# Performance work log

Measured on AMD Instinct MI355X. Metric: run time of the kernel, lower is better.

## Reference

```python
import jax, jax.numpy as jnp
import numpy as np

B, T, DIM = 8, 1024, 512
H, DK, L = 8, 64, 32          # heads, dim_key, rel_pos_length
DH = H * DK                    # dim_hidden = 512
DOUT = 512
EPS = 1e-5


def setup_inputs() -> dict:
    key = jax.random.key(0)
    ks = jax.random.split(key, 5)
    x = jax.random.normal(ks[0], (B, T, DIM), jnp.float32)
    Wqkv = jax.random.normal(ks[1], (3 * DH, DIM), jnp.float32) * (1.0 / np.sqrt(DIM))
    Wout = jax.random.normal(ks[2], (DOUT, DH), jnp.float32) * (1.0 / np.sqrt(DH))
    bout = jax.random.normal(ks[3], (DOUT,), jnp.float32) * 0.01
    rel_positions = jax.random.normal(ks[4], (2 * L - 1, DK), jnp.float32)
    bn_gamma = jnp.ones((DK,), jnp.float32)
    bn_beta = jnp.zeros((DK,), jnp.float32)
    return {"x": x, "Wqkv": Wqkv, "Wout": Wout, "bout": bout,
            "rel_positions": rel_positions, "bn_gamma": bn_gamma, "bn_beta": bn_beta}


def reference(x, Wqkv, Wout, bout, rel_positions, bn_gamma, bn_beta):
    b, t, f = x.shape
    # Conv1d(dim, 3*dim_hidden, 1, bias=False) on x.transpose(1,2) == pointwise matmul
    qkv = jnp.einsum('btf,of->bot', x, Wqkv)          # (b, 3*DH, t)
    q, k, v = jnp.split(qkv, 3, axis=1)
    q = q.reshape(b * H, DK, t)
    k = k.reshape(b * H, DK, t)
    v = v.reshape(b * H, DK, t)

    # linear-attention core: softmax over sequence for k, tiny DKxDK context
    k = jax.nn.softmax(k, axis=-1)
    context = jnp.einsum('ndt,net->nde', k, v)        # (n, DK, DK)
    content_out = jnp.einsum('nde,ndt->net', context, q)  # (n, DK, t); norm_queries=False

    # Relative-position path. Original builds one-hot It (t,t,2L-1) and
    # Pt = einsum('tir,rd->tid', It, rel_positions); then
    # St = einsum('ndt,tid->nit', q, Pt); rel = einsum('nit,net->net', St, v)
    #     = v * (sum_i St)[:,None,:].
    # sum_i Pt[t,i,d] = sum over valid band offsets of rel_positions -> band matmul.
    r = jnp.arange(-(L - 1), L)                       # (2L-1,)
    pos = jnp.arange(t)
    tgt = pos[:, None] + r[None, :]                   # i = x + r
    valid = ((tgt >= 0) & (tgt < t)).astype(x.dtype)  # (t, 2L-1)
    Psum = valid @ rel_positions                      # (t, DK) == Pt.sum(axis=1)
    S = jnp.einsum('ndt,td->nt', q, Psum)             # (n, t)
    rel = v * S[:, None, :]                           # (n, DK, t)

    # BatchNorm1d(DK), training-mode batch stats over (n, t), biased variance
    mu = jnp.mean(rel, axis=(0, 2), keepdims=True)
    var = jnp.mean((rel - mu) ** 2, axis=(0, 2), keepdims=True)
    rel = (rel - mu) * jax.lax.rsqrt(var + EPS) * bn_gamma[None, :, None] + bn_beta[None, :, None]

    out = (content_out + rel).reshape(b, DH, t)
    # Conv1d(dim_hidden, dim_out, 1) with bias
    return jnp.einsum('od,bdt->bot', Wout, out) + bout[None, :, None]
```

## Files before the change

### kernel.cpp

```cpp
#include <hip/hip_runtime.h>
#include <hip/hip_bf16.h>


typedef short bf16x8 __attribute__((ext_vector_type(8)));
typedef float f32x4 __attribute__((ext_vector_type(4)));

static __device__ __forceinline__ unsigned short f2bf(float f) {
  __hip_bfloat16 h = __float2bfloat16(f);
  return *reinterpret_cast<unsigned short*>(&h);
}
static __device__ __forceinline__ float bf2f(unsigned short u) {
  union { unsigned int i; float f; } c; c.i = ((unsigned int)u) << 16;
  return c.f;
}
static __device__ __forceinline__ void gl_lds16(const unsigned short* g, unsigned short* l) {
  __builtin_amdgcn_global_load_lds((const __attribute__((address_space(1))) unsigned int*)g,
                                   (__attribute__((address_space(3))) unsigned int*)l,
                                   16, 0, 0);
}

__global__ __launch_bounds__(256) void prep(const float* __restrict__ x,
                                            const float* __restrict__ wqkv,
                                            const float* __restrict__ wout,
                                            const float* __restrict__ relpos,
                                            unsigned short* __restrict__ xb,
                                            unsigned short* __restrict__ wqkvb,
                                            unsigned short* __restrict__ woutb,
                                            float* __restrict__ PsumT) {
  const int bx = blockIdx.x;
  if (bx < 5120) {
    int j = bx * 256 + threadIdx.x;
    const float* src; unsigned short* dst;
    if (j < 1048576) { src = x; dst = xb; }
    else if (j < 1245184) { j -= 1048576; src = wqkv; dst = wqkvb; }
    else { j -= 1245184; src = wout; dst = woutb; }
    float4 v = ((const float4*)src)[j];
    ushort4 o = {f2bf(v.x), f2bf(v.y), f2bf(v.z), f2bf(v.w)};
    ((ushort4*)dst)[j] = o;
  } else {
    const int idx = bx - 5120;
    const int d = idx >> 2;
    const int t = (idx & 3) * 256 + threadIdx.x;
    float acc = 0.f;
    for (int j = 0; j < 63; ++j) {
      int i = t + j - 31;
      float v = relpos[j * 64 + d];
      if (i >= 0 && i < 1024) acc += v;
    }
    PsumT[d * 1024 + t] = acc;
  }
}


__global__ __launch_bounds__(256) void gemm_qkv(const unsigned short* __restrict__ A,
                                                const unsigned short* __restrict__ B,
                                                unsigned short* __restrict__ C) {
  __shared__ alignas(16) unsigned short As[8192];
  __shared__ alignas(16) unsigned short Bs[8192];
  const int tid = threadIdx.x;
  const int wave = tid >> 6, lane = tid & 63;
  const int bm = blockIdx.y * 128, bn = blockIdx.x * 128;
  const int wm = (wave >> 1) * 64, wn = (wave & 1) * 64;
  const int fr = lane & 15, cq = lane >> 4;
  const unsigned short* srcA[4];
  const unsigned short* srcB[4];
#pragma unroll
  for (int j = 0; j < 4; ++j) {
    const int s = tid + j * 256;
    const int row = s >> 3, cp = s & 7;
    const int c = cp ^ (row & 7);
    srcA[j] = A + (size_t)(bm + row) * 512 + c * 8;
    srcB[j] = B + (size_t)(bn + row) * 512 + c * 8;
  }
  int offA[4][2], offB[4][2];
#pragma unroll
  for (int i = 0; i < 4; ++i)
#pragma unroll
    for (int ks = 0; ks < 2; ++ks) {
      int ra = wm + i * 16 + fr;
      offA[i][ks] = (ra * 8 + ((ks * 4 + cq) ^ (ra & 7))) * 8;
      int rb = wn + i * 16 + fr;
      offB[i][ks] = (rb * 8 + ((ks * 4 + cq) ^ (rb & 7))) * 8;
    }
  f32x4 acc[4][4];
#pragma unroll
  for (int i = 0; i < 4; ++i)
#pragma unroll
    for (int j = 0; j < 4; ++j) acc[i][j] = (f32x4){0.f, 0.f, 0.f, 0.f};
  for (int k0 = 0; k0 < 512; k0 += 64) {
    __syncthreads();
#pragma unroll
    for (int j = 0; j < 4; ++j) {
      gl_lds16(srcA[j] + k0, As + (wave * 64 + j * 256) * 8);
      gl_lds16(srcB[j] + k0, Bs + (wave * 64 + j * 256) * 8);
    }
    __builtin_amdgcn_s_waitcnt(0);
    __syncthreads();
#pragma unroll
    for (int ks = 0; ks < 2; ++ks) {
      bf16x8 af[4], bq[4];
#pragma unroll
      for (int mi = 0; mi < 4; ++mi) af[mi] = *(const bf16x8*)(As + offA[mi][ks]);
#pragma unroll
      for (int nj = 0; nj < 4; ++nj) bq[nj] = *(const bf16x8*)(Bs + offB[nj][ks]);
#pragma unroll
      for (int mi = 0; mi < 4; ++mi)
#pragma unroll
        for (int nj = 0; nj < 4; ++nj)
          acc[mi][nj] = __builtin_amdgcn_mfma_f32_16x16x32_bf16(af[mi], bq[nj], acc[mi][nj], 0, 0, 0);
    }
  }
#pragma unroll
  for (int mi = 0; mi < 4; ++mi) {
    const int row0 = bm + wm + mi * 16 + (lane >> 4) * 4;
#pragma unroll
    for (int nj = 0; nj < 4; ++nj) {
      const int col = bn + wn + nj * 16 + fr;
#pragma unroll
      for (int rr = 0; rr < 4; ++rr)
        C[(size_t)(row0 + rr) * 8192 + col] = f2bf(acc[mi][nj][rr]);
    }
  }
}

__global__ __launch_bounds__(256) void gemm_out(const unsigned short* __restrict__ A,
                                                const unsigned short* __restrict__ B,
                                                const float* __restrict__ bias,
                                                float* __restrict__ out) {
  __shared__ alignas(16) unsigned short As[8192];
  __shared__ alignas(16) unsigned short Bs[8192];
  const int tid = threadIdx.x;
  const int wave = tid >> 6, lane = tid & 63;
  const int bm = blockIdx.y * 128, bn = blockIdx.x * 128;
  const int wm = (wave >> 1) * 64, wn = (wave & 1) * 64;
  const int fr = lane & 15, cq = lane >> 4;
  const unsigned short* srcA[4];
  const unsigned short* srcB[4];
#pragma unroll
  for (int j = 0; j < 4; ++j) {
    const int s = tid + j * 256;
    const int row = s >> 3, cp = s & 7;
    const int c = cp ^ (row & 7);
    srcA[j] = A + (size_t)(bm + row) * 512 + c * 8;
    srcB[j] = B + (size_t)(bn + row) * 512 + c * 8;
  }
  int offA[4][2], offB[4][2];
#pragma unroll
  for (int i = 0; i < 4; ++i)
#pragma unroll
    for (int ks = 0; ks < 2; ++ks) {
      int ra = wm + i * 16 + fr;
      offA[i][ks] = (ra * 8 + ((ks * 4 + cq) ^ (ra & 7))) * 8;
      int rb = wn + i * 16 + fr;
      offB[i][ks] = (rb * 8 + ((ks * 4 + cq) ^ (rb & 7))) * 8;
    }
  f32x4 acc[4][4];
#pragma unroll
  for (int i = 0; i < 4; ++i)
#pragma unroll
    for (int j = 0; j < 4; ++j) acc[i][j] = (f32x4){0.f, 0.f, 0.f, 0.f};
  for (int k0 = 0; k0 < 512; k0 += 64) {
    __syncthreads();
#pragma unroll
    for (int j = 0; j < 4; ++j) {
      gl_lds16(srcA[j] + k0, As + (wave * 64 + j * 256) * 8);
      gl_lds16(srcB[j] + k0, Bs + (wave * 64 + j * 256) * 8);
    }
    __builtin_amdgcn_s_waitcnt(0);
    __syncthreads();
#pragma unroll
    for (int ks = 0; ks < 2; ++ks) {
      bf16x8 af[4], bq[4];
#pragma unroll
      for (int mi = 0; mi < 4; ++mi) af[mi] = *(const bf16x8*)(As + offA[mi][ks]);
#pragma unroll
      for (int nj = 0; nj < 4; ++nj) bq[nj] = *(const bf16x8*)(Bs + offB[nj][ks]);
#pragma unroll
      for (int mi = 0; mi < 4; ++mi)
#pragma unroll
        for (int nj = 0; nj < 4; ++nj)
          acc[mi][nj] = __builtin_amdgcn_mfma_f32_16x16x32_bf16(af[mi], bq[nj], acc[mi][nj], 0, 0, 0);
    }
  }
#pragma unroll
  for (int mi = 0; mi < 4; ++mi) {
    const int row0 = bm + wm + mi * 16 + (lane >> 4) * 4;
#pragma unroll
    for (int nj = 0; nj < 4; ++nj) {
      const int col = bn + wn + nj * 16 + fr;
      const int b = col >> 10, t = col & 1023;
#pragma unroll
      for (int rr = 0; rr < 4; ++rr)
        out[(size_t)b * 524288 + (size_t)(row0 + rr) * 1024 + t] = acc[mi][nj][rr] + bias[row0 + rr];
    }
  }
}

__global__ __launch_bounds__(256) void stats(const unsigned short* __restrict__ qkv,
                                             const float* __restrict__ PsumT,
                                             float* __restrict__ S,
                                             float* __restrict__ part1,
                                             float* __restrict__ part2,
                                             float* __restrict__ lse) {
  const int bx = blockIdx.x;
  const int tid = threadIdx.x, wave = tid >> 6, lane = tid & 63;
  __shared__ float swave[4][64];
  __shared__ float s_lds[64];
  if (bx < 1024) {
    const int tc = bx & 15, n = bx >> 4;
    const int b = n >> 3, h = n & 7;
    const int t0 = tc * 64;
    const int tg = lane & 7, rg = lane >> 3;
    const unsigned short* qbase = qkv + (size_t)(h * 64) * 8192 + b * 1024 + t0 + tg * 8;
    const float* pbase = PsumT + t0 + tg * 8;
    float acc[8] = {0.f};
#pragma unroll
    for (int i = 0; i < 2; ++i) {
      const int d = wave * 16 + i * 8 + rg;
      bf16x8 qv = *(const bf16x8*)(qbase + (size_t)d * 8192);
      float4 p0 = *(const float4*)(pbase + d * 1024);
      float4 p1 = *(const float4*)(pbase + d * 1024 + 4);
      float p[8] = {p0.x, p0.y, p0.z, p0.w, p1.x, p1.y, p1.z, p1.w};
#pragma unroll
      for (int j = 0; j < 8; ++j) acc[j] = fmaf(bf2f((unsigned short)qv[j]), p[j], acc[j]);
    }
#pragma unroll
    for (int off = 8; off < 64; off <<= 1)
#pragma unroll
      for (int j = 0; j < 8; ++j) acc[j] += __shfl_xor(acc[j], off);
    if (rg == 0) {
#pragma unroll
      for (int j = 0; j < 8; ++j) swave[wave][tg * 8 + j] = acc[j];
    }
    __syncthreads();
    if (tid < 64) {
      float s = swave[0][tid] + swave[1][tid] + swave[2][tid] + swave[3][tid];
      s_lds[tid] = s;
      S[(size_t)n * 1024 + t0 + tid] = s;
    }
    __syncthreads();
    const unsigned short* vbase = qkv + (size_t)(1024 + h * 64) * 8192 + b * 1024 + t0 + tg * 8;
    const int blk = n * 16 + tc;
    float sv[8];
#pragma unroll
    for (int j = 0; j < 8; ++j) sv[j] = s_lds[tg * 8 + j];
#pragma unroll
    for (int i = 0; i < 2; ++i) {
      const int e = wave * 16 + i * 8 + rg;
      bf16x8 vv = *(const bf16x8*)(vbase + (size_t)e * 8192);
      float a1 = 0.f, a2 = 0.f;
#pragma unroll
      for (int j = 0; j < 8; ++j) {
        float val = bf2f((unsigned short)vv[j]) * sv[j];
        a1 += val;
        a2 = fmaf(val, val, a2);
      }
#pragma unroll
      for (int off = 1; off < 8; off <<= 1) {
        a1 += __shfl_xor(a1, off);
        a2 += __shfl_xor(a2, off);
      }
      if (tg == 0) {
        part1[e * 1024 + blk] = a1;
        part2[e * 1024 + blk] = a2;
      }
    }
  } else {
    const int r = (bx - 1024) * 4 + wave;
    const int hd = r >> 3, b = r & 7;
    const unsigned short* row = qkv + (size_t)(512 + hd) * 8192 + b * 1024 + lane * 16;
    uint4 u0 = *(const uint4*)row;
    uint4 u1 = *(const uint4*)(row + 8);
    const unsigned short* us0 = (const unsigned short*)&u0;
    const unsigned short* us1 = (const unsigned short*)&u1;
    float f[16];
#pragma unroll
    for (int i = 0; i < 8; ++i) { f[i] = bf2f(us0[i]); f[8 + i] = bf2f(us1[i]); }
    float m = f[0];
#pragma unroll
    for (int i = 1; i < 16; ++i) m = fmaxf(m, f[i]);
#pragma unroll
    for (int off = 32; off; off >>= 1) m = fmaxf(m, __shfl_xor(m, off));
    float s = 0.f;
#pragma unroll
    for (int i = 0; i < 16; ++i) s += __expf(f[i] - m);
#pragma unroll
    for (int off = 32; off; off >>= 1) s += __shfl_xor(s, off);
    if (lane == 0) lse[r] = m + __logf(s);
  }
}

__global__ __launch_bounds__(256) void context_mfma(const unsigned short* __restrict__ qkv,
                                                    const float* __restrict__ lse,
                                                    float* __restrict__ ctx_part) {
  const int tc = blockIdx.x, n = blockIdx.y;
  const int b = n >> 3, h = n & 7;
  const int tid = threadIdx.x;
  const int wave = tid >> 6, lane = tid & 63;
  __shared__ float ls[64];
  __shared__ float ctx_l[64][68];
  if (tid < 64) ls[tid] = lse[(h * 64 + tid) * 8 + b];
  __syncthreads();
  const int fr = lane & 15, fk = (lane >> 4) * 8;
  const size_t colbase = (size_t)b * 1024 + tc * 256 + wave * 64;
  const unsigned short* kbase = qkv + (size_t)(512 + h * 64) * 8192 + colbase;
  const unsigned short* vbase = qkv + (size_t)(1024 + h * 64) * 8192 + colbase;
  f32x4 acc[4][4];
#pragma unroll
  for (int i = 0; i < 4; ++i)
#pragma unroll
    for (int j = 0; j < 4; ++j) acc[i][j] = (f32x4){0.f, 0.f, 0.f, 0.f};
#pragma unroll
  for (int ks = 0; ks < 2; ++ks) {
    const int tb = ks * 32 + fk;
    bf16x8 aF[4], bF[4];
#pragma unroll
    for (int dt = 0; dt < 4; ++dt) {
      const int row = dt * 16 + fr;
      bf16x8 kv = *(const bf16x8*)(kbase + (size_t)row * 8192 + tb);
      const float lv = ls[row];
      bf16x8 pv;
#pragma unroll
      for (int j = 0; j < 8; ++j)
        pv[j] = (short)f2bf(__expf(bf2f((unsigned short)kv[j]) - lv));
      aF[dt] = pv;
    }
#pragma unroll
    for (int et = 0; et < 4; ++et)
      bF[et] = *(const bf16x8*)(vbase + (size_t)(et * 16 + fr) * 8192 + tb);
#pragma unroll
    for (int dt = 0; dt < 4; ++dt)
#pragma unroll
      for (int et = 0; et < 4; ++et)
        acc[dt][et] = __builtin_amdgcn_mfma_f32_16x16x32_bf16(aF[dt], bF[et], acc[dt][et], 0, 0, 0);
  }
#pragma unroll
  for (int w = 0; w < 4; ++w) {
    if (wave == w) {
#pragma unroll
      for (int dt = 0; dt < 4; ++dt)
#pragma unroll
        for (int et = 0; et < 4; ++et) {
          const int col = et * 16 + fr;
#pragma unroll
          for (int rr = 0; rr < 4; ++rr) {
            const int rw = dt * 16 + (lane >> 4) * 4 + rr;
            if (w == 0) ctx_l[rw][col] = acc[dt][et][rr];
            else ctx_l[rw][col] += acc[dt][et][rr];
          }
        }
    }
    __syncthreads();
  }
  float* outp = ctx_part + ((size_t)tc * 64 + n) * 4096;
  for (int i = tid * 4; i < 4096; i += 1024) {
    const int rw = i >> 6, cc = i & 63;
    *(float4*)(outp + i) = *(const float4*)&ctx_l[rw][cc];
  }
}

__global__ __launch_bounds__(256) void reduce2(const float* __restrict__ part,
                                               float* __restrict__ ctx,
                                               const float* __restrict__ part1,
                                               const float* __restrict__ part2,
                                               const float* __restrict__ gamma,
                                               const float* __restrict__ beta,
                                               float* __restrict__ scale,
                                               float* __restrict__ shift) {
  const int bx = blockIdx.x;
  const int tid = threadIdx.x;
  if (bx < 256) {
    const int i4 = bx * 256 + tid;
    const float4* p = (const float4*)part;
    float4 a = p[i4], b = p[65536 + i4], c = p[131072 + i4], d = p[196608 + i4];
    float4 s = {a.x + b.x + c.x + d.x, a.y + b.y + c.y + d.y,
                a.z + b.z + c.z + d.z, a.w + b.w + c.w + d.w};
    ((float4*)ctx)[i4] = s;
  } else {
    const int e = bx - 256;
    float a1 = 0.f, a2 = 0.f;
#pragma unroll
    for (int i = 0; i < 4; ++i) {
      a1 += part1[e * 1024 + i * 256 + tid];
      a2 += part2[e * 1024 + i * 256 + tid];
    }
#pragma unroll
    for (int off = 32; off; off >>= 1) {
      a1 += __shfl_down(a1, off);
      a2 += __shfl_down(a2, off);
    }
    __shared__ float r1[4], r2[4];
    const int w = tid >> 6, lane = tid & 63;
    if (lane == 0) { r1[w] = a1; r2[w] = a2; }
    __syncthreads();
    if (tid == 0) {
      float s1 = r1[0] + r1[1] + r1[2] + r1[3];
      float s2 = r2[0] + r2[1] + r2[2] + r2[3];
      const float cnt = 65536.0f;
      float mu = s1 / cnt;
      float var = s2 / cnt - mu * mu;
      float sc = gamma[e] * rsqrtf(var + 1e-5f);
      scale[e] = sc;
      shift[e] = beta[e] - mu * sc;
    }
  }
}

__global__ __launch_bounds__(256) void content_out_t(const unsigned short* __restrict__ qkv,
                                                     const float* __restrict__ ctx,
                                                     const float* __restrict__ S,
                                                     const float* __restrict__ scale,
                                                     const float* __restrict__ shift,
                                                     unsigned short* __restrict__ outT) {
  const int chunk = blockIdx.x, n = blockIdx.y;
  const int b = n >> 3, h = n & 7;
  const int t0 = chunk * 64;
  __shared__ float cs[4096];
  __shared__ alignas(16) unsigned short T[64][72];
  const float* cp = ctx + (size_t)n * 4096;
  for (int i = threadIdx.x * 4; i < 4096; i += 1024)
    *(float4*)&cs[i] = *(const float4*)&cp[i];
  __syncthreads();
  const int tid = threadIdx.x;
  const int e0 = (tid & 15) * 4;
  const int tq = (tid >> 4) * 4;
  const unsigned short* qbase = qkv + (size_t)(h * 64) * 8192 + b * 1024 + t0 + tq;
  float acc[4][4] = {{0.f}};
  for (int d = 0; d < 64; ++d) {
    float4 cv = *(const float4*)&cs[d * 64 + e0];
    ushort4 qu = *(const ushort4*)(qbase + (size_t)d * 8192);
    float qa[4] = {bf2f(qu.x), bf2f(qu.y), bf2f(qu.z), bf2f(qu.w)};
    float ca[4] = {cv.x, cv.y, cv.z, cv.w};
#pragma unroll
    for (int a = 0; a < 4; ++a)
#pragma unroll
      for (int c = 0; c < 4; ++c)
        acc[a][c] = fmaf(ca[a], qa[c], acc[a][c]);
  }
  float4 svv = *(const float4*)(S + (size_t)n * 1024 + t0 + tq);
  float sa[4] = {svv.x, svv.y, svv.z, svv.w};
  float4 scv = *(const float4*)(scale + e0);
  float4 shv = *(const float4*)(shift + e0);
  float sc[4] = {scv.x, scv.y, scv.z, scv.w};
  float sh[4] = {shv.x, shv.y, shv.z, shv.w};
#pragma unroll
  for (int a = 0; a < 4; ++a) {
    ushort4 vu = *(const ushort4*)(qkv + (size_t)(1024 + h * 64 + e0 + a) * 8192 + b * 1024 + t0 + tq);
    float va[4] = {bf2f(vu.x), bf2f(vu.y), bf2f(vu.z), bf2f(vu.w)};
#pragma unroll
    for (int c = 0; c < 4; ++c)
      T[tq + c][e0 + a] = f2bf(fmaf(va[c] * sa[c], sc[a], acc[a][c] + sh[a]));
  }
  __syncthreads();
  const int tl = tid >> 2, dq = (tid & 3) * 16;
  uint4 r0 = *(uint4*)&T[tl][dq];
  uint4 r1 = *(uint4*)&T[tl][dq + 8];
  unsigned short* op = outT + ((size_t)(b * 1024 + t0 + tl)) * 512 + h * 64 + dq;
  *(uint4*)op = r0;
  *(uint4*)(op + 8) = r1;
}

extern "C" void kernel_launch(void* const* d_in, const int* in_sizes, int n_in,
                              void* d_out, int out_size, void* d_ws, size_t ws_size,
                              hipStream_t stream) {
  const float* x       = (const float*)d_in[0];
  const float* Wqkv    = (const float*)d_in[1];
  const float* Wout    = (const float*)d_in[2];
  const float* bout    = (const float*)d_in[3];
  const float* relpos  = (const float*)d_in[4];
  const float* gamma   = (const float*)d_in[5];
  const float* beta    = (const float*)d_in[6];
  float* out = (float*)d_out;

  float* ws = (float*)d_ws;
  unsigned short* qkvb  = (unsigned short*)ws;
  float* p = ws + 6291456;
  unsigned short* xb    = (unsigned short*)p;  p += 2097152;
  unsigned short* wqkvb = (unsigned short*)p;  p += 393216;
  unsigned short* woutb = (unsigned short*)p;  p += 131072;
  float* ctx_part = p;  p += 1048576;
  float* ctx      = p;  p += 262144;
  float* PsumT    = p;  p += 65536;
  float* S        = p;  p += 65536;
  float* lse      = p;  p += 4096;
  float* part1    = p;  p += 65536;
  float* part2    = p;  p += 65536;
  float* scale    = p;  p += 64;
  float* shift    = p;  p += 64;
  unsigned short* outT = (unsigned short*)p;

  prep<<<5376, 256, 0, stream>>>(x, Wqkv, Wout, relpos, xb, wqkvb, woutb, PsumT);
  gemm_qkv<<<dim3(64, 12), 256, 0, stream>>>(wqkvb, xb, qkvb);
  stats<<<2048, 256, 0, stream>>>(qkvb, PsumT, S, part1, part2, lse);
  context_mfma<<<dim3(4, 64), 256, 0, stream>>>(qkvb, lse, ctx_part);
  reduce2<<<320, 256, 0, stream>>>(ctx_part, ctx, part1, part2, gamma, beta, scale, shift);
  content_out_t<<<dim3(16, 64), 256, 0, stream>>>(qkvb, ctx, S, scale, shift, outT);
  gemm_out<<<dim3(64, 4), 256, 0, stream>>>(woutb, outT, bout, out);
}
```

Before: 163.3 us.

## Fuse softmax-LSE, context MFMA and S computation into one kernel per head quarter

Replaces the stats, context_mfma and reduce2 kernels with ctx_s_kernel and bn_chan. ctx_s_kernel stages a 16-row slice of K in LDS, computes the log-sum-exp and exp in place, and runs the context MFMA over the full sequence. It also accumulates S with atomics into a buffer that prep now zeroes. This removes the ctx_part partial buffer, the lse and part buffers, and a launch. The costs are only 256 blocks for the fused work, a 64-block BN-statistics kernel that rereads V serially, and float atomics that make S summation order nondeterministic.

Result: slower. 171.7 us (+5.1%).

```diff
diff --git a/kernel.cpp b/kernel.cpp
--- a/kernel.cpp
+++ b/kernel.cpp
@@ -26,7 +26,8 @@
                                             unsigned short* __restrict__ xb,
                                             unsigned short* __restrict__ wqkvb,
                                             unsigned short* __restrict__ woutb,
-                                            float* __restrict__ PsumT) {
+                                            float* __restrict__ PsumT,
+                                            float* __restrict__ S) {
   const int bx = blockIdx.x;
   if (bx < 5120) {
     int j = bx * 256 + threadIdx.x;
@@ -37,7 +38,7 @@
     float4 v = ((const float4*)src)[j];
     ushort4 o = {f2bf(v.x), f2bf(v.y), f2bf(v.z), f2bf(v.w)};
     ((ushort4*)dst)[j] = o;
-  } else {
+  } else if (bx < 5376) {
     const int idx = bx - 5120;
     const int d = idx >> 2;
     const int t = (idx & 3) * 256 + threadIdx.x;
@@ -48,9 +49,11 @@
       if (i >= 0 && i < 1024) acc += v;
     }
     PsumT[d * 1024 + t] = acc;
-  }
-}
-
+  } else {
+    const int idx = (bx - 5376) * 256 + threadIdx.x;
+    ((float4*)S)[idx] = (float4){0.f, 0.f, 0.f, 0.f};
+  }
+}
 
 __global__ __launch_bounds__(256) void gemm_qkv(const unsigned short* __restrict__ A,
                                                 const unsigned short* __restrict__ B,
@@ -196,213 +199,157 @@
   }
 }
 
-__global__ __launch_bounds__(256) void stats(const unsigned short* __restrict__ qkv,
-                                             const float* __restrict__ PsumT,
-                                             float* __restrict__ S,
-                                             float* __restrict__ part1,
-                                             float* __restrict__ part2,
-                                             float* __restrict__ lse) {
+__global__ __launch_bounds__(256) void ctx_s_kernel(const unsigned short* __restrict__ qkv,
+                                                    const float* __restrict__ PsumT,
+                                                    float* __restrict__ S,
+                                                    float* __restrict__ ctx) {
   const int bx = blockIdx.x;
+  const int n = (bx & 7) | ((bx >> 5) << 3);
+  const int dq = (bx >> 3) & 3;
+  const int b = n >> 3, h = n & 7;
   const int tid = threadIdx.x, wave = tid >> 6, lane = tid & 63;
-  __shared__ float swave[4][64];
-  __shared__ float s_lds[64];
-  if (bx < 1024) {
-    const int tc = bx & 15, n = bx >> 4;
-    const int b = n >> 3, h = n & 7;
-    const int t0 = tc * 64;
-    const int tg = lane & 7, rg = lane >> 3;
-    const unsigned short* qbase = qkv + (size_t)(h * 64) * 8192 + b * 1024 + t0 + tg * 8;
-    const float* pbase = PsumT + t0 + tg * 8;
-    float acc[8] = {0.f};
-#pragma unroll
-    for (int i = 0; i < 2; ++i) {
-      const int d = wave * 16 + i * 8 + rg;
-      bf16x8 qv = *(const bf16x8*)(qbase + (size_t)d * 8192);
-      float4 p0 = *(const float4*)(pbase + d * 1024);
-      float4 p1 = *(const float4*)(pbase + d * 1024 + 4);
-      float p[8] = {p0.x, p0.y, p0.z, p0.w, p1.x, p1.y, p1.z, p1.w};
-#pragma unroll
-      for (int j = 0; j < 8; ++j) acc[j] = fmaf(bf2f((unsigned short)qv[j]), p[j], acc[j]);
-    }
-#pragma unroll
-    for (int off = 8; off < 64; off <<= 1)
-#pragma unroll
-      for (int j = 0; j < 8; ++j) acc[j] += __shfl_xor(acc[j], off);
-    if (rg == 0) {
-#pragma unroll
-      for (int j = 0; j < 8; ++j) swave[wave][tg * 8 + j] = acc[j];
-    }
-    __syncthreads();
-    if (tid < 64) {
-      float s = swave[0][tid] + swave[1][tid] + swave[2][tid] + swave[3][tid];
-      s_lds[tid] = s;
-      S[(size_t)n * 1024 + t0 + tid] = s;
-    }
-    __syncthreads();
-    const unsigned short* vbase = qkv + (size_t)(1024 + h * 64) * 8192 + b * 1024 + t0 + tg * 8;
-    const int blk = n * 16 + tc;
-    float sv[8];
-#pragma unroll
-    for (int j = 0; j < 8; ++j) sv[j] = s_lds[tg * 8 + j];
-#pragma unroll
-    for (int i = 0; i < 2; ++i) {
-      const int e = wave * 16 + i * 8 + rg;
-      bf16x8 vv = *(const bf16x8*)(vbase + (size_t)e * 8192);
-      float a1 = 0.f, a2 = 0.f;
-#pragma unroll
-      for (int j = 0; j < 8; ++j) {
-        float val = bf2f((unsigned short)vv[j]) * sv[j];
-        a1 += val;
-        a2 = fmaf(val, val, a2);
-      }
-#pragma unroll
-      for (int off = 1; off < 8; off <<= 1) {
-        a1 += __shfl_xor(a1, off);
-        a2 += __shfl_xor(a2, off);
-      }
-      if (tg == 0) {
-        part1[e * 1024 + blk] = a1;
-        part2[e * 1024 + blk] = a2;
-      }
-    }
-  } else {
-    const int r = (bx - 1024) * 4 + wave;
-    const int hd = r >> 3, b = r & 7;
-    const unsigned short* row = qkv + (size_t)(512 + hd) * 8192 + b * 1024 + lane * 16;
-    uint4 u0 = *(const uint4*)row;
-    uint4 u1 = *(const uint4*)(row + 8);
-    const unsigned short* us0 = (const unsigned short*)&u0;
-    const unsigned short* us1 = (const unsigned short*)&u1;
-    float f[16];
-#pragma unroll
-    for (int i = 0; i < 8; ++i) { f[i] = bf2f(us0[i]); f[8 + i] = bf2f(us1[i]); }
-    float m = f[0];
-#pragma unroll
-    for (int i = 1; i < 16; ++i) m = fmaxf(m, f[i]);
+  const int quad = lane >> 4, fr = lane & 15;
+  __shared__ alignas(16) unsigned short kp[16][1028];
+  __shared__ float ls[16];
+  __shared__ float ctx_l[16][68];
+  const unsigned short* kbase = qkv + (size_t)(512 + h * 64 + dq * 16) * 8192 + b * 1024;
+#pragma unroll
+  for (int it = 0; it < 8; ++it) {
+    const int idx = it * 2048 + tid * 8;
+    const int row = idx >> 10, col = idx & 1023;
+    bf16x8 val = *(const bf16x8*)(kbase + (size_t)row * 8192 + col);
+    *(bf16x8*)&kp[row][col] = val;
+  }
+  {
+    const unsigned short* qbase = qkv + (size_t)(h * 64 + dq * 16) * 8192 + b * 1024
+                                  + wave * 256 + lane * 4;
+    const float* pb = PsumT + (dq * 16) * 1024 + wave * 256 + lane * 4;
+    float s0 = 0.f, s1 = 0.f, s2 = 0.f, s3 = 0.f;
+#pragma unroll
+    for (int d = 0; d < 16; ++d) {
+      ushort4 qv = *(const ushort4*)(qbase + (size_t)d * 8192);
+      float4 pv = *(const float4*)(pb + d * 1024);
+      s0 = fmaf(bf2f(qv.x), pv.x, s0);
+      s1 = fmaf(bf2f(qv.y), pv.y, s1);
+      s2 = fmaf(bf2f(qv.z), pv.z, s2);
+      s3 = fmaf(bf2f(qv.w), pv.w, s3);
+    }
+    float* sp = S + (size_t)n * 1024 + wave * 256 + lane * 4;
+    atomicAdd(sp + 0, s0);
+    atomicAdd(sp + 1, s1);
+    atomicAdd(sp + 2, s2);
+    atomicAdd(sp + 3, s3);
+  }
+  __syncthreads();
+#pragma unroll
+  for (int r4 = 0; r4 < 4; ++r4) {
+    const int row = wave * 4 + r4;
+    bf16x8 v0 = *(const bf16x8*)&kp[row][lane * 16];
+    bf16x8 v1 = *(const bf16x8*)&kp[row][lane * 16 + 8];
+    float fv[16];
+#pragma unroll
+    for (int j = 0; j < 8; ++j) {
+      fv[j] = bf2f((unsigned short)v0[j]);
+      fv[8 + j] = bf2f((unsigned short)v1[j]);
+    }
+    float m = fv[0];
+#pragma unroll
+    for (int j = 1; j < 16; ++j) m = fmaxf(m, fv[j]);
 #pragma unroll
     for (int off = 32; off; off >>= 1) m = fmaxf(m, __shfl_xor(m, off));
     float s = 0.f;
 #pragma unroll
-    for (int i = 0; i < 16; ++i) s += __expf(f[i] - m);
+    for (int j = 0; j < 16; ++j) s += __expf(fv[j] - m);
 #pragma unroll
     for (int off = 32; off; off >>= 1) s += __shfl_xor(s, off);
-    if (lane == 0) lse[r] = m + __logf(s);
-  }
-}
-
-__global__ __launch_bounds__(256) void context_mfma(const unsigned short* __restrict__ qkv,
-                                                    const float* __restrict__ lse,
-                                                    float* __restrict__ ctx_part) {
-  const int tc = blockIdx.x, n = blockIdx.y;
-  const int b = n >> 3, h = n & 7;
-  const int tid = threadIdx.x;
-  const int wave = tid >> 6, lane = tid & 63;
-  __shared__ float ls[64];
-  __shared__ float ctx_l[64][68];
-  if (tid < 64) ls[tid] = lse[(h * 64 + tid) * 8 + b];
-  __syncthreads();
-  const int fr = lane & 15, fk = (lane >> 4) * 8;
-  const size_t colbase = (size_t)b * 1024 + tc * 256 + wave * 64;
-  const unsigned short* kbase = qkv + (size_t)(512 + h * 64) * 8192 + colbase;
-  const unsigned short* vbase = qkv + (size_t)(1024 + h * 64) * 8192 + colbase;
-  f32x4 acc[4][4];
-#pragma unroll
-  for (int i = 0; i < 4; ++i)
-#pragma unroll
-    for (int j = 0; j < 4; ++j) acc[i][j] = (f32x4){0.f, 0.f, 0.f, 0.f};
-#pragma unroll
-  for (int ks = 0; ks < 2; ++ks) {
-    const int tb = ks * 32 + fk;
-    bf16x8 aF[4], bF[4];
-#pragma unroll
-    for (int dt = 0; dt < 4; ++dt) {
-      const int row = dt * 16 + fr;
-      bf16x8 kv = *(const bf16x8*)(kbase + (size_t)row * 8192 + tb);
-      const float lv = ls[row];
-      bf16x8 pv;
-#pragma unroll
-      for (int j = 0; j < 8; ++j)
-        pv[j] = (short)f2bf(__expf(bf2f((unsigned short)kv[j]) - lv));
-      aF[dt] = pv;
-    }
-#pragma unroll
-    for (int et = 0; et < 4; ++et)
-      bF[et] = *(const bf16x8*)(vbase + (size_t)(et * 16 + fr) * 8192 + tb);
-#pragma unroll
-    for (int dt = 0; dt < 4; ++dt)
+    if (lane == 0) ls[row] = m + __logf(s);
+  }
+  __syncthreads();
+#pragma unroll
+  for (int it = 0; it < 8; ++it) {
+    const int idx = it * 2048 + tid * 8;
+    const int row = idx >> 10, col = idx & 1023;
+    const float lv = ls[row];
+    bf16x8 kv = *(bf16x8*)&kp[row][col];
+    bf16x8 pv;
+#pragma unroll
+    for (int j = 0; j < 8; ++j)
+      pv[j] = (short)f2bf(__expf(bf2f((unsigned short)kv[j]) - lv));
+    *(bf16x8*)&kp[row][col] = pv;
+  }
+  __syncthreads();
+  f32x4 acc[4];
+#pragma unroll
+  for (int et = 0; et < 4; ++et) acc[et] = (f32x4){0.f, 0.f, 0.f, 0.f};
+  const unsigned short* vbase = qkv + (size_t)(1024 + h * 64) * 8192 + b * 1024 + wave * 256;
+#pragma unroll
+  for (int ks = 0; ks < 8; ++ks) {
+    const int tb = wave * 256 + ks * 32 + quad * 8;
+    bf16x8 aF = *(const bf16x8*)&kp[fr][tb];
+#pragma unroll
+    for (int et = 0; et < 4; ++et) {
+      bf16x8 bF = *(const bf16x8*)(vbase + (size_t)(et * 16 + fr) * 8192 + ks * 32 + quad * 8);
+      acc[et] = __builtin_amdgcn_mfma_f32_16x16x32_bf16(aF, bF, acc[et], 0, 0, 0);
+    }
+  }
+#pragma unroll
+  for (int w2 = 0; w2 < 4; ++w2) {
+    if (wave == w2) {
 #pragma unroll
       for (int et = 0; et < 4; ++et)
-        acc[dt][et] = __builtin_amdgcn_mfma_f32_16x16x32_bf16(aF[dt], bF[et], acc[dt][et], 0, 0, 0);
-  }
-#pragma unroll
-  for (int w = 0; w < 4; ++w) {
-    if (wave == w) {
-#pragma unroll
-      for (int dt = 0; dt < 4; ++dt)
-#pragma unroll
-        for (int et = 0; et < 4; ++et) {
-          const int col = et * 16 + fr;
-#pragma unroll
-          for (int rr = 0; rr < 4; ++rr) {
-            const int rw = dt * 16 + (lane >> 4) * 4 + rr;
-            if (w == 0) ctx_l[rw][col] = acc[dt][et][rr];
-            else ctx_l[rw][col] += acc[dt][et][rr];
-          }
+#pragma unroll
+        for (int rr = 0; rr < 4; ++rr) {
+          const int rd = quad * 4 + rr, ce = et * 16 + fr;
+          if (w2 == 0) ctx_l[rd][ce] = acc[et][rr];
+          else ctx_l[rd][ce] += acc[et][rr];
         }
     }
     __syncthreads();
   }
-  float* outp = ctx_part + ((size_t)tc * 64 + n) * 4096;
-  for (int i = tid * 4; i < 4096; i += 1024) {
-    const int rw = i >> 6, cc = i & 63;
-    *(float4*)(outp + i) = *(const float4*)&ctx_l[rw][cc];
-  }
-}
-
-__global__ __launch_bounds__(256) void reduce2(const float* __restrict__ part,
-                                               float* __restrict__ ctx,
-                                               const float* __restrict__ part1,
-                                               const float* __restrict__ part2,
+  const int idx = tid * 4;
+  const int rd = idx >> 6, ce = idx & 63;
+  float4 val = *(const float4*)&ctx_l[rd][ce];
+  *(float4*)(ctx + (size_t)n * 4096 + (size_t)(dq * 16 + rd) * 64 + ce) = val;
+}
+
+__global__ __launch_bounds__(256) void bn_chan(const unsigned short* __restrict__ qkv,
+                                               const float* __restrict__ S,
                                                const float* __restrict__ gamma,
                                                const float* __restrict__ beta,
                                                float* __restrict__ scale,
                                                float* __restrict__ shift) {
-  const int bx = blockIdx.x;
-  const int tid = threadIdx.x;
-  if (bx < 256) {
-    const int i4 = bx * 256 + tid;
-    const float4* p = (const float4*)part;
-    float4 a = p[i4], b = p[65536 + i4], c = p[131072 + i4], d = p[196608 + i4];
-    float4 s = {a.x + b.x + c.x + d.x, a.y + b.y + c.y + d.y,
-                a.z + b.z + c.z + d.z, a.w + b.w + c.w + d.w};
-    ((float4*)ctx)[i4] = s;
-  } else {
-    const int e = bx - 256;
-    float a1 = 0.f, a2 = 0.f;
-#pragma unroll
-    for (int i = 0; i < 4; ++i) {
-      a1 += part1[e * 1024 + i * 256 + tid];
-      a2 += part2[e * 1024 + i * 256 + tid];
-    }
-#pragma unroll
-    for (int off = 32; off; off >>= 1) {
-      a1 += __shfl_down(a1, off);
-      a2 += __shfl_down(a2, off);
-    }
-    __shared__ float r1[4], r2[4];
-    const int w = tid >> 6, lane = tid & 63;
-    if (lane == 0) { r1[w] = a1; r2[w] = a2; }
-    __syncthreads();
-    if (tid == 0) {
-      float s1 = r1[0] + r1[1] + r1[2] + r1[3];
-      float s2 = r2[0] + r2[1] + r2[2] + r2[3];
-      const float cnt = 65536.0f;
-      float mu = s1 / cnt;
-      float var = s2 / cnt - mu * mu;
-      float sc = gamma[e] * rsqrtf(var + 1e-5f);
-      scale[e] = sc;
-      shift[e] = beta[e] - mu * sc;
-    }
+  const int e = blockIdx.x, tid = threadIdx.x;
+  float a1 = 0.f, a2 = 0.f;
+  for (int n = 0; n < 64; ++n) {
+    const int b = n >> 3, h = n & 7;
+    ushort4 vv = *(const ushort4*)(qkv + (size_t)(1024 + h * 64 + e) * 8192 + b * 1024 + tid * 4);
+    float4 sv = *(const float4*)(S + (size_t)n * 1024 + tid * 4);
+    float v0 = bf2f(vv.x) * sv.x;
+    float v1 = bf2f(vv.y) * sv.y;
+    float v2 = bf2f(vv.z) * sv.z;
+    float v3 = bf2f(vv.w) * sv.w;
+    a1 += v0 + v1 + v2 + v3;
+    a2 = fmaf(v0, v0, a2); a2 = fmaf(v1, v1, a2);
+    a2 = fmaf(v2, v2, a2); a2 = fmaf(v3, v3, a2);
+  }
+#pragma unroll
+  for (int off = 32; off; off >>= 1) {
+    a1 += __shfl_down(a1, off);
+    a2 += __shfl_down(a2, off);
+  }
+  __shared__ float r1[4], r2[4];
+  const int w = tid >> 6, lane = tid & 63;
+  if (lane == 0) { r1[w] = a1; r2[w] = a2; }
+  __syncthreads();
+  if (tid == 0) {
+    float s1 = r1[0] + r1[1] + r1[2] + r1[3];
+    float s2 = r2[0] + r2[1] + r2[2] + r2[3];
+    const float cnt = 65536.0f;
+    float mu = s1 / cnt;
+    float var = s2 / cnt - mu * mu;
+    float sc = gamma[e] * rsqrtf(var + 1e-5f);
+    scale[e] = sc;
+    shift[e] = beta[e] - mu * sc;
   }
 }
 
@@ -478,22 +425,17 @@
   unsigned short* xb    = (unsigned short*)p;  p += 2097152;
   unsigned short* wqkvb = (unsigned short*)p;  p += 393216;
   unsigned short* woutb = (unsigned short*)p;  p += 131072;
-  float* ctx_part = p;  p += 1048576;
   float* ctx      = p;  p += 262144;
   float* PsumT    = p;  p += 65536;
   float* S        = p;  p += 65536;
-  float* lse      = p;  p += 4096;
-  float* part1    = p;  p += 65536;
-  float* part2    = p;  p += 65536;
   float* scale    = p;  p += 64;
   float* shift    = p;  p += 64;
   unsigned short* outT = (unsigned short*)p;
 
-  prep<<<5376, 256, 0, stream>>>(x, Wqkv, Wout, relpos, xb, wqkvb, woutb, PsumT);
+  prep<<<5440, 256, 0, stream>>>(x, Wqkv, Wout, relpos, xb, wqkvb, woutb, PsumT, S);
   gemm_qkv<<<dim3(64, 12), 256, 0, stream>>>(wqkvb, xb, qkvb);
-  stats<<<2048, 256, 0, stream>>>(qkvb, PsumT, S, part1, part2, lse);
-  context_mfma<<<dim3(4, 64), 256, 0, stream>>>(qkvb, lse, ctx_part);
-  reduce2<<<320, 256, 0, stream>>>(ctx_part, ctx, part1, part2, gamma, beta, scale, shift);
+  ctx_s_kernel<<<256, 256, 0, stream>>>(qkvb, PsumT, S, ctx);
+  bn_chan<<<64, 256, 0, stream>>>(qkvb, S, gamma, beta, scale, shift);
   content_out_t<<<dim3(16, 64), 256, 0, stream>>>(qkvb, ctx, S, scale, shift, outT);
   gemm_out<<<dim3(64, 4), 256, 0, stream>>>(woutb, outT, bout, out);
 }
```
